# Performance work log

Measured on AMD Instinct MI355X. Metric: run time of the kernel, lower is better.

## Reference

```python
import jax, jax.numpy as jnp
import numpy as np

B, N, C = 64, 256, 512
SHIFTS = (-1, 0, 1)
# torch.chunk(N, 3): ceil(256/3)=86 -> sizes [86, 86, 84]
CHUNK_SIZES = (86, 86, 84)
EPS = 1e-5


def _shift_pad(a, s):
    # shift along last axis (C) with zero padding, matching shift_with_padding
    if s == 0:
        return a
    if s > 0:
        return jnp.pad(a[..., :-s], ((0, 0), (0, 0), (s, 0)))
    s = -s
    return jnp.pad(a[..., s:], ((0, 0), (0, 0), (0, s)))


def setup_inputs() -> dict:
    key = jax.random.key(0)
    ks = jax.random.split(key, 16)
    w = lambda k, shape: (jax.random.normal(k, shape, jnp.float32) * 0.02)
    inp = {
        "x": jax.random.normal(ks[0], (B, N, C), jnp.float32),
        "ln_g": jnp.ones((C,), jnp.float32),
        "ln_b": jnp.zeros((C,), jnp.float32),
        "Ws": w(ks[1], (C, C)),
        "bs": jnp.zeros((C,), jnp.float32),
        "Wc": w(ks[2], (N, N, 3)),     # Conv1d weight [out=N, in=N, k=3]
        "bc": jnp.zeros((N,), jnp.float32),
        "We1": w(ks[3], (N, N // 8)),
        "be1": jnp.zeros((N // 8,), jnp.float32),
        "We2": w(ks[4], (N // 8, N)),
        "be2": jnp.zeros((N,), jnp.float32),
        "Wf1": w(ks[5], (C, 2 * C)),
        "bf1": jnp.zeros((2 * C,), jnp.float32),
        "Wf2": w(ks[6], (2 * C, C)),
        "bf2": jnp.zeros((C,), jnp.float32),
    }
    return inp


def reference(x, ln_g, ln_b, Ws, bs, Wc, bc, We1, be1, We2, be2, Wf1, bf1, Wf2, bf2):
    res = x
    # channel_mixer_S: LayerNorm over C, then Linear C->C + relu (dropout=0)
    mu = jnp.mean(x, axis=-1, keepdims=True)
    var = jnp.mean((x - mu) ** 2, axis=-1, keepdims=True)
    h = (x - mu) * jax.lax.rsqrt(var + EPS) * ln_g + ln_b
    h = jax.nn.relu(h @ Ws + bs)                      # [B, N, C]
    # channel_shift: chunk along N, shift each chunk along C with zero pad
    offs = np.cumsum((0,) + CHUNK_SIZES)
    chunks = [h[:, offs[i]:offs[i + 1], :] for i in range(3)]
    x_shift = jnp.concatenate([_shift_pad(c, s) for c, s in zip(chunks, SHIFTS)], axis=1)
    # channel_projection: Conv1d over C with N channels, k=3, pad=1
    x_shift = jax.lax.conv_general_dilated(
        x_shift, Wc, window_strides=(1,), padding=[(1, 1)],
        dimension_numbers=("NCH", "OIH", "NCH")) + bc[None, :, None]
    # SE gating
    se = jnp.mean(x_shift, axis=-1)                   # [B, N]
    ex = jax.nn.sigmoid(jax.nn.relu(se @ We1 + be1) @ We2 + be2)  # [B, N]
    z = x_shift * ex[:, :, None]
    # channel_mixer_F: C -> 2C (relu) -> C, residual
    z = jax.nn.relu(z @ Wf1 + bf1) @ Wf2 + bf2 + res
    return z
```

## Files before the change

kernel.cpp:

```cpp
#include <hip/hip_runtime.h>
#include <hip/hip_bf16.h>
#include <math.h>

#define BB 64
#define NN 256
#define CCH 512

typedef unsigned short u16;
typedef __attribute__((ext_vector_type(8))) short s16x8;
typedef __attribute__((ext_vector_type(4))) float f32x4;

#define AS1 __attribute__((address_space(1)))
#define AS3 __attribute__((address_space(3)))

static __device__ __forceinline__ u16 f2b(float f) {
    __hip_bfloat16 h = __float2bfloat16(f);
    union { __hip_bfloat16 h; u16 u; } x; x.h = h; return x.u;
}
static __device__ __forceinline__ void gll16(const void* g, void* l) {
    __builtin_amdgcn_global_load_lds((const AS1 unsigned int*)g,
                                     (AS3 unsigned int*)l, 16, 0, 0);
}
static __device__ __forceinline__ int shf(int ni) {
    return (ni < 86) ? -1 : (ni < 172 ? 0 : 1);
}

#define VM8  asm volatile("s_waitcnt vmcnt(8)" ::: "memory")
#define VM4  asm volatile("s_waitcnt vmcnt(4)" ::: "memory")
#define VM0  asm volatile("s_waitcnt vmcnt(0)" ::: "memory")
#define MEMB asm volatile("" ::: "memory")

static __device__ __forceinline__ void wtc_body(const float* __restrict__ W,
    u16* __restrict__ Wt, int K, int N, int bx, int by, float* t, bool perm)
{
    int n0 = bx * 32, k0 = by * 32;
    int tx = threadIdx.x & 31, ty = threadIdx.x >> 5;
    #pragma unroll
    for (int i = 0; i < 4; ++i)
        t[(ty + i * 8) * 33 + tx] = W[(size_t)(k0 + ty + i * 8) * N + n0 + tx];
    __syncthreads();
    int kl = k0 + tx;
    int kp = perm ? ((kl & ~63) | ((kl & 15) << 2) | ((kl >> 4) & 3)) : kl;
    #pragma unroll
    for (int i = 0; i < 4; ++i)
        Wt[(size_t)(n0 + ty + i * 8) * K + kp] = f2b(t[tx * 33 + ty + i * 8]);
}

__global__ __launch_bounds__(256) void prep_ln_kernel(
    const float* __restrict__ Ws,  u16* __restrict__ Wst,
    const float* __restrict__ Wf1, u16* __restrict__ Wf1t,
    const float* __restrict__ Wf2, u16* __restrict__ Wf2t,
    const float* __restrict__ Wc,  u16* __restrict__ Wc3,
    u16* __restrict__ Hts,
    const float* __restrict__ x, const float* __restrict__ g,
    const float* __restrict__ bta, u16* __restrict__ xnorm)
{
    __shared__ float t[32 * 33];
    int bid = blockIdx.x;
    if (bid < 256) {
        wtc_body(Ws, Wst, 512, 512, bid & 15, bid >> 4, t, false);
    } else if (bid < 768) {
        int idx = bid - 256;
        wtc_body(Wf1, Wf1t, 512, 1024, idx & 31, idx >> 5, t, true);
    } else if (bid < 1280) {
        int idx = bid - 768;
        wtc_body(Wf2, Wf2t, 1024, 512, idx & 15, idx >> 4, t, true);
    } else if (bid < 2048) {
        int idx = (bid - 1280) * 256 + threadIdx.x;
        int xloc = idx & 255;
        int o = (idx >> 8) & 255;
        int k = idx >> 16;
        int il = (xloc & ~63) | ((xloc & 63) >> 2) | ((xloc & 3) << 4);
        Wc3[idx] = f2b(Wc[((size_t)o * NN + il) * 3 + k]);
    } else if (bid < 2304) {
        int idx = (bid - 2048) * 256 + threadIdx.x;
        int b   = idx >> 10;
        int rem = idx & 1023;
        int rr  = rem >> 8;
        int r   = (rr & 1) + (rr >> 1) * 512;
        Hts[((size_t)b * 514 + r) * 256 + (rem & 255)] = 0;
    } else {
        const int l = threadIdx.x & 63;
        const int r = (bid - 2304) * 4 + (threadIdx.x >> 6);
        const float4* xr = (const float4*)(x + (size_t)r * CCH);
        float4 v1 = xr[l];
        float4 v2 = xr[l + 64];
        float s  = v1.x + v1.y + v1.z + v1.w + v2.x + v2.y + v2.z + v2.w;
        float ss = v1.x*v1.x + v1.y*v1.y + v1.z*v1.z + v1.w*v1.w
                 + v2.x*v2.x + v2.y*v2.y + v2.z*v2.z + v2.w*v2.w;
        #pragma unroll
        for (int o = 32; o > 0; o >>= 1) {
            s  += __shfl_xor(s, o);
            ss += __shfl_xor(ss, o);
        }
        float mu  = s * (1.0f / CCH);
        float var = ss * (1.0f / CCH) - mu * mu;
        float rs  = rsqrtf(var + 1e-5f);
        float4 g1 = ((const float4*)g)[l],   g2 = ((const float4*)g)[l + 64];
        float4 b1 = ((const float4*)bta)[l], b2 = ((const float4*)bta)[l + 64];
        ushort4 o1, o2;
        o1.x = f2b((v1.x - mu) * rs * g1.x + b1.x);
        o1.y = f2b((v1.y - mu) * rs * g1.y + b1.y);
        o1.z = f2b((v1.z - mu) * rs * g1.z + b1.z);
        o1.w = f2b((v1.w - mu) * rs * g1.w + b1.w);
        o2.x = f2b((v2.x - mu) * rs * g2.x + b2.x);
        o2.y = f2b((v2.y - mu) * rs * g2.y + b2.y);
        o2.z = f2b((v2.z - mu) * rs * g2.z + b2.z);
        o2.w = f2b((v2.w - mu) * rs * g2.w + b2.w);
        ushort4* orow = (ushort4*)(xnorm + (size_t)r * CCH);
        orow[l]      = o1;
        orow[l + 64] = o2;
    }
}

template<int MODE>
__global__ __launch_bounds__(256, 2) void gemm_pipe(
    const u16* __restrict__ A, const u16* __restrict__ Bt,
    const float* __restrict__ bias, const float* __restrict__ res,
    void* __restrict__ outv, u16* __restrict__ auxout,
    float* __restrict__ SEpart, const float* __restrict__ EX)
{
    constexpr int NK = (MODE == 2) ? 32 : (MODE == 3) ? 24 : 16;
    constexpr int SA = (MODE == 2) ? 1024 : 512;
    constexpr int SB = (MODE == 2) ? 1024 : 512;

    __shared__ u16 Asm[4 * 4096];
    __shared__ u16 Bsm[4 * 4096];

    const int tid = threadIdx.x;
    const int l   = tid & 63;
    const int w   = tid >> 6;
    const int nwg = gridDim.x;
    const int work = (blockIdx.x & 7) * (nwg >> 3) + (blockIdx.x >> 3);

    int row0, col0, bidx = 0;
    if (MODE == 0)      { row0 = (work >> 7) * 128; col0 = (work & 127) * 128; }
    else if (MODE == 1) { row0 = (work >> 3) * 128; col0 = (work & 7) * 128; }
    else if (MODE == 2) { row0 = (work >> 2) * 128; col0 = (work & 3) * 128; }
    else                { bidx = work >> 3; row0 = ((work >> 2) & 1) * 128;
                          col0 = (work & 3) * 128; }

    const u16* Aab  = A + (size_t)row0 * SA;
    const u16* Bab  = Bt + (size_t)col0 * SB;
    const u16* HtsB = Bt + (size_t)bidx * 514 * 256;

    const int wm = (w >> 1) * 64;
    const int wn = (w & 1) * 64;
    const int fr = l & 15;
    const int q  = l >> 4;
    const int kofs = ((q ^ ((l >> 1) & 3)) * 8);

    const f32x4 zero = {0.0f, 0.0f, 0.0f, 0.0f};
    f32x4 acc[4][4];
    #pragma unroll
    for (int m = 0; m < 4; ++m)
        #pragma unroll
        for (int n = 0; n < 4; ++n) acc[m][n] = zero;

    const int kc0 = ((tid & 3) ^ ((tid >> 3) & 3)) * 8;
    const int srow = tid >> 2;

    auto stage = [&](int u, int slot) {
        u16* ald = Asm + slot * 4096 + w * 512;
        u16* bld = Bsm + slot * 4096 + w * 512;
        if (MODE == 3) {
            const int kseg = u >> 3, kb = (u & 7) * 32 + kc0;
            gll16(A + kseg * 65536 + (row0 + srow) * 256 + kb, ald);
            gll16(A + kseg * 65536 + (row0 + srow + 64) * 256 + kb, ald + 2048);
            gll16(HtsB + (size_t)(col0 + srow + kseg) * 256 + kb, bld);
            gll16(HtsB + (size_t)(col0 + srow + 64 + kseg) * 256 + kb, bld + 2048);
        } else {
            const int kb = u * 32 + kc0;
            gll16(Aab + (size_t)srow * SA + kb, ald);
            gll16(Aab + (size_t)(srow + 64) * SA + kb, ald + 2048);
            gll16(Bab + (size_t)srow * SB + kb, bld);
            gll16(Bab + (size_t)(srow + 64) * SB + kb, bld + 2048);
        }
    };

    stage(0, 0); stage(1, 1); stage(2, 2);
    for (int u = 0; u < NK; ++u) {
        if (u < NK - 2)       { VM8; }
        else if (u == NK - 2) { VM4; }
        else                  { VM0; }
        __builtin_amdgcn_s_barrier();
        MEMB;
        const int slot = u & 3;
        s16x8 bf4[4], af[4];
        #pragma unroll
        for (int n = 0; n < 4; ++n)
            bf4[n] = *(const s16x8*)&Bsm[slot * 4096 + (wn + n * 16 + fr) * 32 + kofs];
        #pragma unroll
        for (int m = 0; m < 4; ++m)
            af[m] = *(const s16x8*)&Asm[slot * 4096 + (wm + m * 16 + fr) * 32 + kofs];
        if (u + 3 < NK) stage(u + 3, (u + 3) & 3);
        __builtin_amdgcn_s_setprio(1);
        #pragma unroll
        for (int m = 0; m < 4; ++m)
            #pragma unroll
            for (int n = 0; n < 4; ++n)
                acc[m][n] = __builtin_amdgcn_mfma_f32_16x16x32_bf16(af[m], bf4[n], acc[m][n], 0, 0, 0);
        __builtin_amdgcn_s_setprio(0);
        MEMB;
    }

    if (MODE == 0) {
        const int gb = col0 + wn;
        const int b  = gb >> 8;
        const int gl = gb & 255;
        const int nib = gl + fr;
        u16* HtsW = auxout + (size_t)b * 514 * 256;
        const int px = gl + 4 * fr;
        const int s0 = shf(nib), s3 = shf(nib + 48);
        #pragma unroll
        for (int m = 0; m < 4; ++m) {
            #pragma unroll
            for (int j = 0; j < 4; ++j) {
                const int c = row0 + wm + m * 16 + q * 4 + j;
                const float bsv = bias[c];
                u16 vv[4];
                #pragma unroll
                for (int n = 0; n < 4; ++n)
                    vv[n] = f2b(fmaxf(acc[m][n][j] + bsv, 0.0f));
                if (s0 == s3) {
                    ushort4 v4 = {vv[0], vv[1], vv[2], vv[3]};
                    *(ushort4*)&HtsW[(size_t)(c + 1 + s0) * 256 + px] = v4;
                } else {
                    #pragma unroll
                    for (int n = 0; n < 4; ++n)
                        HtsW[(size_t)(c + 1 + shf(nib + n * 16)) * 256 + px + n] = vv[n];
                }
            }
        }
    } else if (MODE == 1) {
        const int cgb = col0 + wn;
        float bval[4];
        #pragma unroll
        for (int n = 0; n < 4; ++n) bval[n] = bias[cgb + n * 16 + fr];
        #pragma unroll
        for (int m = 0; m < 4; ++m) {
            #pragma unroll
            for (int j = 0; j < 4; ++j) {
                const int row = row0 + wm + m * 16 + q * 4 + j;
                const float sc = EX[row];
                u16 vv[4];
                #pragma unroll
                for (int n = 0; n < 4; ++n)
                    vv[n] = f2b(fmaxf(acc[m][n][j] * sc + bval[n], 0.0f));
                ushort4 v4 = {vv[0], vv[1], vv[2], vv[3]};
                *(ushort4*)&((u16*)outv)[(size_t)row * 1024 + cgb + 4 * fr] = v4;
            }
        }
    } else if (MODE == 2) {
        #pragma unroll
        for (int m = 0; m < 4; ++m) {
            #pragma unroll
            for (int j = 0; j < 4; ++j) {
                const int row = row0 + wm + m * 16 + q * 4 + j;
                #pragma unroll
                for (int n = 0; n < 4; ++n) {
                    const int col = col0 + wn + n * 16 + fr;
                    ((float*)outv)[(size_t)row * 512 + col] =
                        acc[m][n][j] + bias[col] + res[(size_t)row * 512 + col];
                }
            }
        }
    } else {
        const int cb = col0 + wn;
        const int px = cb + 4 * fr;
        const int sslot = cb >> 6;
        #pragma unroll
        for (int m = 0; m < 4; ++m) {
            #pragma unroll
            for (int j = 0; j < 4; ++j) {
                const int no = row0 + wm + m * 16 + q * 4 + j;
                const float bcv = bias[no];
                float p = 0.0f;
                u16 vv[4];
                #pragma unroll
                for (int n = 0; n < 4; ++n) {
                    float v = acc[m][n][j];
                    vv[n] = f2b(v + bcv);
                    p += v;
                }
                ushort4 v4 = {vv[0], vv[1], vv[2], vv[3]};
                *(ushort4*)&auxout[((size_t)bidx * NN + no) * CCH + px] = v4;
                p += __shfl_xor(p, 1);
                p += __shfl_xor(p, 2);
                p += __shfl_xor(p, 4);
                p += __shfl_xor(p, 8);
                if (fr == 0)
                    SEpart[sslot * 16384 + bidx * NN + no] = p;
            }
        }
    }
}

__global__ __launch_bounds__(256) void semlp_kernel(const float* __restrict__ sep,
    const float* __restrict__ bc,
    const float* __restrict__ We1, const float* __restrict__ be1,
    const float* __restrict__ We2, const float* __restrict__ be2,
    float* __restrict__ ex)
{
    __shared__ float sse[256];
    __shared__ float e1[32];
    int b = blockIdx.x, t = threadIdx.x;
    int o = b * 256 + t;
    float sum = 0.0f;
    #pragma unroll
    for (int i = 0; i < 8; ++i) sum += sep[i * 16384 + o];
    sse[t] = sum * (1.0f / CCH) + bc[t];
    __syncthreads();
    if (t < 32) {
        float a = be1[t];
        #pragma unroll 8
        for (int i = 0; i < 256; ++i) a += sse[i] * We1[i * 32 + t];
        e1[t] = fmaxf(a, 0.0f);
    }
    __syncthreads();
    float a = be2[t];
    #pragma unroll
    for (int j = 0; j < 32; ++j) a += e1[j] * We2[j * 256 + t];
    ex[b * 256 + t] = 1.0f / (1.0f + expf(-a));
}

extern "C" void kernel_launch(void* const* d_in, const int* in_sizes, int n_in,
                              void* d_out, int out_size, void* d_ws, size_t ws_size,
                              hipStream_t stream) {
    const float* x    = (const float*)d_in[0];
    const float* ln_g = (const float*)d_in[1];
    const float* ln_b = (const float*)d_in[2];
    const float* Ws   = (const float*)d_in[3];
    const float* bs   = (const float*)d_in[4];
    const float* Wc   = (const float*)d_in[5];
    const float* bc   = (const float*)d_in[6];
    const float* We1  = (const float*)d_in[7];
    const float* be1  = (const float*)d_in[8];
    const float* We2  = (const float*)d_in[9];
    const float* be2  = (const float*)d_in[10];
    const float* Wf1  = (const float*)d_in[11];
    const float* bf1  = (const float*)d_in[12];
    const float* Wf2  = (const float*)d_in[13];
    const float* bf2  = (const float*)d_in[14];
    float* out = (float*)d_out;
    char* w8   = (char*)d_ws;

    u16* XN  = (u16*)(w8);
    u16* Y   = XN;
    u16* Hts = (u16*)(w8 + (16u << 20));
    u16* T   = (u16*)(w8 + (16u << 20));
    char* tail = w8 + 50397184;
    float* SEpart = (float*)(tail);
    u16* Wst      = (u16*)(tail + 524288);
    u16* Wf1t     = (u16*)(tail + 1048576);
    u16* Wf2t     = (u16*)(tail + 2097152);
    u16* Wc3      = (u16*)(tail + 3145728);
    float* EX     = (float*)(tail + 3538944);

    prep_ln_kernel<<<6400, 256, 0, stream>>>(Ws, Wst, Wf1, Wf1t, Wf2, Wf2t,
                                             Wc, Wc3, Hts, x, ln_g, ln_b, XN);
    gemm_pipe<0><<<512, 256, 0, stream>>>(Wst, XN, bs, nullptr,
        nullptr, Hts, nullptr, nullptr);
    gemm_pipe<3><<<512, 256, 0, stream>>>(Wc3, Hts, bc, nullptr,
        nullptr, Y, SEpart, nullptr);
    semlp_kernel<<<BB, 256, 0, stream>>>(SEpart, bc, We1, be1, We2, be2, EX);
    gemm_pipe<1><<<1024, 256, 0, stream>>>(Y, Wf1t, bf1, nullptr,
        T, nullptr, nullptr, EX);
    gemm_pipe<2><<<512, 256, 0, stream>>>(T, Wf2t, bf2, x,
        out, nullptr, nullptr, nullptr);
}
```

Measured before the change: 117.5 us.

## Use 256x128 tiles with 8 waves and a 6-slot pipeline; add double-buffered FFN1 GEMM

The three GEMM modes (S-mixer, conv, FFN2) now use 512-thread blocks with 256x128 output tiles and a 6-slot LDS ring. Each iteration consumes two K-steps and prefetches two more, so B tiles are reused across twice as many rows and there are fewer barriers per K-step. The FFN1 GEMM moves to a separate kernel with a 2-slot double buffer and 4 blocks per CU, trading pipeline depth for occupancy. Risks are lower occupancy and more LDS for the big-tile kernels, plus index changes in the SE-partial slot mapping and the conv row mapping.

New measurement: 116.8 us. About the same (-0.6%).

```diff
diff --git a/kernel.cpp b/kernel.cpp
--- a/kernel.cpp
+++ b/kernel.cpp
@@ -25,8 +25,7 @@
     return (ni < 86) ? -1 : (ni < 172 ? 0 : 1);
 }
 
-#define VM8  asm volatile("s_waitcnt vmcnt(8)" ::: "memory")
-#define VM4  asm volatile("s_waitcnt vmcnt(4)" ::: "memory")
+#define VM6  asm volatile("s_waitcnt vmcnt(6)" ::: "memory")
 #define VM0  asm volatile("s_waitcnt vmcnt(0)" ::: "memory")
 #define MEMB asm volatile("" ::: "memory")
 
@@ -114,18 +113,18 @@
 }
 
 template<int MODE>
-__global__ __launch_bounds__(256, 2) void gemm_pipe(
+__global__ __launch_bounds__(512, 1) void gemm_pipe(
     const u16* __restrict__ A, const u16* __restrict__ Bt,
     const float* __restrict__ bias, const float* __restrict__ res,
     void* __restrict__ outv, u16* __restrict__ auxout,
-    float* __restrict__ SEpart, const float* __restrict__ EX)
+    float* __restrict__ SEpart)
 {
     constexpr int NK = (MODE == 2) ? 32 : (MODE == 3) ? 24 : 16;
     constexpr int SA = (MODE == 2) ? 1024 : 512;
     constexpr int SB = (MODE == 2) ? 1024 : 512;
 
-    __shared__ u16 Asm[4 * 4096];
-    __shared__ u16 Bsm[4 * 4096];
+    __shared__ u16 Asm[6 * 8192];
+    __shared__ u16 Bsm[6 * 4096];
 
     const int tid = threadIdx.x;
     const int l   = tid & 63;
@@ -134,11 +133,9 @@
     const int work = (blockIdx.x & 7) * (nwg >> 3) + (blockIdx.x >> 3);
 
     int row0, col0, bidx = 0;
-    if (MODE == 0)      { row0 = (work >> 7) * 128; col0 = (work & 127) * 128; }
-    else if (MODE == 1) { row0 = (work >> 3) * 128; col0 = (work & 7) * 128; }
-    else if (MODE == 2) { row0 = (work >> 2) * 128; col0 = (work & 3) * 128; }
-    else                { bidx = work >> 3; row0 = ((work >> 2) & 1) * 128;
-                          col0 = (work & 3) * 128; }
+    if (MODE == 0)      { row0 = (work >> 7) * 256; col0 = (work & 127) * 128; }
+    else if (MODE == 2) { row0 = (work >> 2) * 256; col0 = (work & 3) * 128; }
+    else                { row0 = 0; bidx = work >> 2; col0 = (work & 3) * 128; }
 
     const u16* Aab  = A + (size_t)row0 * SA;
     const u16* Bab  = Bt + (size_t)col0 * SB;
@@ -161,47 +158,66 @@
     const int srow = tid >> 2;
 
     auto stage = [&](int u, int slot) {
-        u16* ald = Asm + slot * 4096 + w * 512;
+        u16* ald = Asm + slot * 8192 + w * 512;
         u16* bld = Bsm + slot * 4096 + w * 512;
         if (MODE == 3) {
             const int kseg = u >> 3, kb = (u & 7) * 32 + kc0;
-            gll16(A + kseg * 65536 + (row0 + srow) * 256 + kb, ald);
-            gll16(A + kseg * 65536 + (row0 + srow + 64) * 256 + kb, ald + 2048);
+            gll16(A + kseg * 65536 + srow * 256 + kb, ald);
+            gll16(A + kseg * 65536 + (srow + 128) * 256 + kb, ald + 4096);
             gll16(HtsB + (size_t)(col0 + srow + kseg) * 256 + kb, bld);
-            gll16(HtsB + (size_t)(col0 + srow + 64 + kseg) * 256 + kb, bld + 2048);
         } else {
             const int kb = u * 32 + kc0;
             gll16(Aab + (size_t)srow * SA + kb, ald);
-            gll16(Aab + (size_t)(srow + 64) * SA + kb, ald + 2048);
+            gll16(Aab + (size_t)(srow + 128) * SA + kb, ald + 4096);
             gll16(Bab + (size_t)srow * SB + kb, bld);
-            gll16(Bab + (size_t)(srow + 64) * SB + kb, bld + 2048);
         }
     };
 
-    stage(0, 0); stage(1, 1); stage(2, 2);
-    for (int u = 0; u < NK; ++u) {
-        if (u < NK - 2)       { VM8; }
-        else if (u == NK - 2) { VM4; }
-        else                  { VM0; }
+    stage(0, 0); stage(1, 1); stage(2, 2); stage(3, 3);
+    int sa = 0;
+    constexpr int NV = NK / 2;
+    for (int v = 0; v < NV; ++v) {
+        if (v + 1 < NV) { VM6; } else { VM0; }
         __builtin_amdgcn_s_barrier();
         MEMB;
-        const int slot = u & 3;
-        s16x8 bf4[4], af[4];
+        const int sb = sa + 1;
+        s16x8 b0[4], af0[4];
         #pragma unroll
         for (int n = 0; n < 4; ++n)
-            bf4[n] = *(const s16x8*)&Bsm[slot * 4096 + (wn + n * 16 + fr) * 32 + kofs];
-        #pragma unroll
-        for (int m = 0; m < 4; ++m)
-            af[m] = *(const s16x8*)&Asm[slot * 4096 + (wm + m * 16 + fr) * 32 + kofs];
-        if (u + 3 < NK) stage(u + 3, (u + 3) & 3);
+            b0[n] = *(const s16x8*)&Bsm[sa * 4096 + (wn + n * 16 + fr) * 32 + kofs];
+        #pragma unroll
+        for (int m = 0; m < 4; ++m)
+            af0[m] = *(const s16x8*)&Asm[sa * 8192 + (wm + m * 16 + fr) * 32 + kofs];
+        const int u2 = 2 * v + 4;
+        if (u2 < NK) {
+            int st = sa + 4; if (st >= 6) st -= 6;
+            stage(u2, st);
+            int st1 = st + 1; if (st1 >= 6) st1 -= 6;
+            stage(u2 + 1, st1);
+        }
         __builtin_amdgcn_s_setprio(1);
         #pragma unroll
         for (int m = 0; m < 4; ++m)
             #pragma unroll
             for (int n = 0; n < 4; ++n)
-                acc[m][n] = __builtin_amdgcn_mfma_f32_16x16x32_bf16(af[m], bf4[n], acc[m][n], 0, 0, 0);
+                acc[m][n] = __builtin_amdgcn_mfma_f32_16x16x32_bf16(af0[m], b0[n], acc[m][n], 0, 0, 0);
+        __builtin_amdgcn_s_setprio(0);
+        s16x8 b1[4], af1[4];
+        #pragma unroll
+        for (int n = 0; n < 4; ++n)
+            b1[n] = *(const s16x8*)&Bsm[sb * 4096 + (wn + n * 16 + fr) * 32 + kofs];
+        #pragma unroll
+        for (int m = 0; m < 4; ++m)
+            af1[m] = *(const s16x8*)&Asm[sb * 8192 + (wm + m * 16 + fr) * 32 + kofs];
+        __builtin_amdgcn_s_setprio(1);
+        #pragma unroll
+        for (int m = 0; m < 4; ++m)
+            #pragma unroll
+            for (int n = 0; n < 4; ++n)
+                acc[m][n] = __builtin_amdgcn_mfma_f32_16x16x32_bf16(af1[m], b1[n], acc[m][n], 0, 0, 0);
         __builtin_amdgcn_s_setprio(0);
         MEMB;
+        sa += 2; if (sa >= 6) sa = 0;
     }
 
     if (MODE == 0) {
@@ -232,25 +248,6 @@
                 }
             }
         }
-    } else if (MODE == 1) {
-        const int cgb = col0 + wn;
-        float bval[4];
-        #pragma unroll
-        for (int n = 0; n < 4; ++n) bval[n] = bias[cgb + n * 16 + fr];
-        #pragma unroll
-        for (int m = 0; m < 4; ++m) {
-            #pragma unroll
-            for (int j = 0; j < 4; ++j) {
-                const int row = row0 + wm + m * 16 + q * 4 + j;
-                const float sc = EX[row];
-                u16 vv[4];
-                #pragma unroll
-                for (int n = 0; n < 4; ++n)
-                    vv[n] = f2b(fmaxf(acc[m][n][j] * sc + bval[n], 0.0f));
-                ushort4 v4 = {vv[0], vv[1], vv[2], vv[3]};
-                *(ushort4*)&((u16*)outv)[(size_t)row * 1024 + cgb + 4 * fr] = v4;
-            }
-        }
     } else if (MODE == 2) {
         #pragma unroll
         for (int m = 0; m < 4; ++m) {
@@ -268,12 +265,12 @@
     } else {
         const int cb = col0 + wn;
         const int px = cb + 4 * fr;
-        const int sslot = cb >> 6;
+        const int sslot = (col0 >> 7) * 2 + (wn >> 6);
         #pragma unroll
         for (int m = 0; m < 4; ++m) {
             #pragma unroll
             for (int j = 0; j < 4; ++j) {
-                const int no = row0 + wm + m * 16 + q * 4 + j;
+                const int no = wm + m * 16 + q * 4 + j;
                 const float bcv = bias[no];
                 float p = 0.0f;
                 u16 vv[4];
@@ -292,6 +289,95 @@
                 if (fr == 0)
                     SEpart[sslot * 16384 + bidx * NN + no] = p;
             }
+        }
+    }
+}
+
+__global__ __launch_bounds__(256, 4) void gemm1_hi(
+    const u16* __restrict__ Yb, const u16* __restrict__ Wf1t,
+    const float* __restrict__ bf1, u16* __restrict__ T,
+    const float* __restrict__ EX)
+{
+    __shared__ u16 Asm[2 * 4096];
+    __shared__ u16 Bsm[2 * 4096];
+
+    const int tid = threadIdx.x;
+    const int l   = tid & 63;
+    const int w   = tid >> 6;
+    const int work = (blockIdx.x & 7) * 128 + (blockIdx.x >> 3);
+    const int row0 = (work >> 3) * 128;
+    const int col0 = (work & 7) * 128;
+
+    const u16* Aab = Yb   + (size_t)row0 * 512;
+    const u16* Bab = Wf1t + (size_t)col0 * 512;
+
+    const int wm = (w >> 1) * 64;
+    const int wn = (w & 1) * 64;
+    const int fr = l & 15;
+    const int q  = l >> 4;
+    const int kofs = ((q ^ ((l >> 1) & 3)) * 8);
+
+    const f32x4 zero = {0.0f, 0.0f, 0.0f, 0.0f};
+    f32x4 acc[4][4];
+    #pragma unroll
+    for (int m = 0; m < 4; ++m)
+        #pragma unroll
+        for (int n = 0; n < 4; ++n) acc[m][n] = zero;
+
+    const int kc0 = ((tid & 3) ^ ((tid >> 3) & 3)) * 8;
+    const int srow = tid >> 2;
+
+    auto stage = [&](int u, int slot) {
+        u16* ald = Asm + slot * 4096 + w * 512;
+        u16* bld = Bsm + slot * 4096 + w * 512;
+        const int kb = u * 32 + kc0;
+        gll16(Aab + (size_t)srow * 512 + kb, ald);
+        gll16(Aab + (size_t)(srow + 64) * 512 + kb, ald + 2048);
+        gll16(Bab + (size_t)srow * 512 + kb, bld);
+        gll16(Bab + (size_t)(srow + 64) * 512 + kb, bld + 2048);
+    };
+
+    stage(0, 0);
+    VM0;
+    __builtin_amdgcn_s_barrier();
+    for (int u = 0; u < 16; ++u) {
+        const int slot = u & 1;
+        if (u + 1 < 16) stage(u + 1, slot ^ 1);
+        s16x8 bf4[4], af[4];
+        #pragma unroll
+        for (int n = 0; n < 4; ++n)
+            bf4[n] = *(const s16x8*)&Bsm[slot * 4096 + (wn + n * 16 + fr) * 32 + kofs];
+        #pragma unroll
+        for (int m = 0; m < 4; ++m)
+            af[m] = *(const s16x8*)&Asm[slot * 4096 + (wm + m * 16 + fr) * 32 + kofs];
+        __builtin_amdgcn_s_setprio(1);
+        #pragma unroll
+        for (int m = 0; m < 4; ++m)
+            #pragma unroll
+            for (int n = 0; n < 4; ++n)
+                acc[m][n] = __builtin_amdgcn_mfma_f32_16x16x32_bf16(af[m], bf4[n], acc[m][n], 0, 0, 0);
+        __builtin_amdgcn_s_setprio(0);
+        MEMB;
+        VM0;
+        __builtin_amdgcn_s_barrier();
+    }
+
+    const int cgb = col0 + wn;
+    float bval[4];
+    #pragma unroll
+    for (int n = 0; n < 4; ++n) bval[n] = bf1[cgb + n * 16 + fr];
+    #pragma unroll
+    for (int m = 0; m < 4; ++m) {
+        #pragma unroll
+        for (int j = 0; j < 4; ++j) {
+            const int row = row0 + wm + m * 16 + q * 4 + j;
+            const float sc = EX[row];
+            u16 vv[4];
+            #pragma unroll
+            for (int n = 0; n < 4; ++n)
+                vv[n] = f2b(fmaxf(acc[m][n][j] * sc + bval[n], 0.0f));
+            ushort4 v4 = {vv[0], vv[1], vv[2], vv[3]};
+            *(ushort4*)&T[(size_t)row * 1024 + cgb + 4 * fr] = v4;
         }
     }
 }
@@ -359,13 +445,12 @@
 
     prep_ln_kernel<<<6400, 256, 0, stream>>>(Ws, Wst, Wf1, Wf1t, Wf2, Wf2t,
                                              Wc, Wc3, Hts, x, ln_g, ln_b, XN);
-    gemm_pipe<0><<<512, 256, 0, stream>>>(Wst, XN, bs, nullptr,
-        nullptr, Hts, nullptr, nullptr);
-    gemm_pipe<3><<<512, 256, 0, stream>>>(Wc3, Hts, bc, nullptr,
-        nullptr, Y, SEpart, nullptr);
+    gemm_pipe<0><<<256, 512, 0, stream>>>(Wst, XN, bs, nullptr,
+                                          nullptr, Hts, nullptr);
+    gemm_pipe<3><<<256, 512, 0, stream>>>(Wc3, Hts, bc, nullptr,
+                                          nullptr, Y, SEpart);
     semlp_kernel<<<BB, 256, 0, stream>>>(SEpart, bc, We1, be1, We2, be2, EX);
-    gemm_pipe<1><<<1024, 256, 0, stream>>>(Y, Wf1t, bf1, nullptr,
-        T, nullptr, nullptr, EX);
-    gemm_pipe<2><<<512, 256, 0, stream>>>(T, Wf2t, bf2, x,
-        out, nullptr, nullptr, nullptr);
-}
+    gemm1_hi<<<1024, 256, 0, stream>>>(Y, Wf1t, bf1, T, EX);
+    gemm_pipe<2><<<256, 512, 0, stream>>>(T, Wf2t, bf2, x,
+                                          out, nullptr, nullptr);
+}
```
